# Kernel optimization log

Hardware: AMD Instinct MI355X
Metric: run time of the kernel (lower is better)

Reference implementation:

```python
import jax, jax.numpy as jnp
import numpy as np

N, CH = 65536, 256
B, K, CTX = 8, 256, 768
H, D = 8, 64
NPB = N // B  # points per batch (scene)


def setup_inputs() -> dict:
    key = jax.random.key(0)
    ks = jax.random.split(key, 8)
    xF = jax.random.normal(ks[0], (N, CH), dtype=jnp.float32)
    context = jax.random.normal(ks[1], (B, K, CTX), dtype=jnp.float32)
    # decomposition_permutations: a random partition of the N sparse points into B groups
    perm = jax.random.permutation(ks[2], N).reshape(B, NPB).astype(jnp.int32)
    Wq = jax.random.normal(ks[3], (CH, H * D), dtype=jnp.float32) * 0.02
    Wk = jax.random.normal(ks[4], (CTX, H * D), dtype=jnp.float32) * 0.02
    Wv = jax.random.normal(ks[5], (CTX, H * D), dtype=jnp.float32) * 0.02
    Wout = jax.random.normal(ks[6], (H * D, CH), dtype=jnp.float32) * 0.02
    b_out = jnp.zeros((CH,), dtype=jnp.float32)
    return {"xF": xF, "context": context, "perm": perm,
            "Wq": Wq, "Wk": Wk, "Wv": Wv, "Wout": Wout, "b_out": b_out}


def reference(xF, context, perm, Wq, Wk, Wv, Wout, b_out):
    scale = D ** -0.5
    q = (xF @ Wq).reshape(N, H, D)                     # to_q (1x1 conv == linear)
    k = (context @ Wk).reshape(B, K, H, D)             # to_k
    v = (context @ Wv).reshape(B, K, H, D)             # to_v
    qg = q[perm]                                        # gather: [B, NPB, H, D]
    attn = jax.nn.softmax(scale * jnp.einsum('bqhd,bkhd->bhqk', qg, k), axis=-1)
    o = jnp.einsum('bhqk,bkhd->bqhd', attn, v).reshape(B * NPB, H * D)
    # inverse-permutation scatter back to sparse-tensor order: ft[inv_perm]
    ft = jnp.zeros((N, H * D), o.dtype).at[perm.reshape(-1)].set(o)
    out = ft @ Wout + b_out                             # to_out
    return out + xF                                     # residual
```

## Files before the change

### kernel.cpp

```cpp
#include <hip/hip_runtime.h>

typedef unsigned short u16;
typedef __attribute__((ext_vector_type(8))) short bf16x8;
typedef __attribute__((ext_vector_type(4))) float f32x4;
typedef __attribute__((ext_vector_type(4))) int i32x4;
typedef __attribute__((ext_vector_type(2))) int i32x2;

#define N_PTS   65536
#define CH_DIM  256
#define BATCH   8
#define KTOK    256
#define CTX_DIM 768
#define NHEAD   8
#define HD      64
#define HDIM    512
#define NPB     8192

__device__ __forceinline__ u16 f2bf(float f) {
    union { float f; unsigned u; } v; v.f = f;
    unsigned r = v.u + 0x7fffu + ((v.u >> 16) & 1u);
    return (u16)(r >> 16);
}
__device__ __forceinline__ unsigned pk2bf(float lo, float hi) {
    return (unsigned)f2bf(lo) | ((unsigned)f2bf(hi) << 16);
}

__device__ __forceinline__ void gll16(const void* g, void* l) {
    __builtin_amdgcn_global_load_lds(
        (const __attribute__((address_space(1))) void*)g,
        (__attribute__((address_space(3))) void*)l, 16, 0, 0);
}

__global__ void convk(const float* __restrict__ src, u16* __restrict__ dst, int n8) {
    int i = blockIdx.x * blockDim.x + threadIdx.x;
    int st = gridDim.x * blockDim.x;
    for (; i < n8; i += st) {
        const float* p = src + (size_t)i * 8;
        f32x4 a = *(const f32x4*)p;
        f32x4 b = *(const f32x4*)(p + 4);
        union { u16 h[8]; i32x4 q; } pk;
#pragma unroll
        for (int j = 0; j < 4; j++) { pk.h[j] = f2bf(a[j]); pk.h[4 + j] = f2bf(b[j]); }
        *(i32x4*)&dst[(size_t)i * 8] = pk.q;
    }
}

__global__ void tconvk(const float* __restrict__ W, u16* __restrict__ WT, int R, int C) {
    int i = blockIdx.x * blockDim.x + threadIdx.x;
    if (i >= R * C) return;
    int c = i / R, r = i - c * R;
    WT[(size_t)c * R + r] = f2bf(W[(size_t)r * C + c]);
}

template <bool OUT_F32, bool VT_OUT>
__global__ __launch_bounds__(256, 3) void gemm_bt(
    const u16* __restrict__ A, const u16* __restrict__ BT, void* __restrict__ Cv,
    int M, int N, int K,
    const float* __restrict__ bias, const float* __restrict__ resid, float oscale)
{
    __shared__ __align__(16) u16 As[128 * 32];
    __shared__ __align__(16) u16 Bs[128 * 32];

    const int tid  = threadIdx.x;
    const int lane = tid & 63;
    const int w    = tid >> 6;
    const int wm   = w & 1;
    const int wn   = w >> 1;

    const int nwg = gridDim.x * gridDim.y;
    const int wg  = blockIdx.y * gridDim.x + blockIdx.x;
    const int swz = (wg & 7) * (nwg >> 3) + (wg >> 3);
    const int n0  = (swz % gridDim.x) * 128;
    const int m0  = (swz / gridDim.x) * 128;

    const int l15  = lane & 15;
    const int quad = lane >> 4;

    f32x4 acc[4][4];
#pragma unroll
    for (int i = 0; i < 4; i++)
#pragma unroll
        for (int j = 0; j < 4; j++) { acc[i][j][0]=0.f; acc[i][j][1]=0.f; acc[i][j][2]=0.f; acc[i][j][3]=0.f; }

    const int sr = tid >> 2;
    const int sc = (tid & 3) * 8;
    const u16* Abase = A  + (size_t)(m0 + sr) * K + sc;
    const u16* Bbase = BT + (size_t)(n0 + sr) * K + sc;
    u16* AsD = &As[tid * 8];
    u16* BsD = &Bs[tid * 8];
    const size_t rowStep = (size_t)64 * K;

    for (int k0 = 0; k0 < K; k0 += 32) {
        gll16(Abase + k0,           AsD);
        gll16(Abase + k0 + rowStep, AsD + 2048);
        gll16(Bbase + k0,           BsD);
        gll16(Bbase + k0 + rowStep, BsD + 2048);
        __syncthreads();

        bf16x8 af[4], bfr[4];
#pragma unroll
        for (int rt = 0; rt < 4; rt++)
            af[rt] = *(const bf16x8*)&As[(wm * 64 + rt * 16 + l15) * 32 + quad * 8];
#pragma unroll
        for (int nt = 0; nt < 4; nt++)
            bfr[nt] = *(const bf16x8*)&Bs[(wn * 64 + nt * 16 + l15) * 32 + quad * 8];
#pragma unroll
        for (int rt = 0; rt < 4; rt++)
#pragma unroll
            for (int nt = 0; nt < 4; nt++)
                acc[rt][nt] = __builtin_amdgcn_mfma_f32_16x16x32_bf16(af[rt], bfr[nt], acc[rt][nt], 0, 0, 0);
        __syncthreads();
    }

    if (VT_OUT) {
        u16* CT = (u16*)Cv;
#pragma unroll
        for (int nt = 0; nt < 4; nt++) {
            int col = n0 + wn * 64 + nt * 16 + l15;
            int hh = col >> 6, dd = col & 63;
#pragma unroll
            for (int rt = 0; rt < 4; rt++) {
                int row = m0 + wm * 64 + rt * 16 + quad * 4;
                int bb = row >> 8, jb = row & 255;
                int jp = (jb & 0xE0) | ((jb & 0x0C) << 1) | ((jb & 0x10) >> 2);
                union { u16 h[4]; i32x2 q; } pk;
#pragma unroll
                for (int r = 0; r < 4; r++) pk.h[r] = f2bf(acc[rt][nt][r]);
                *(i32x2*)&CT[(((size_t)(bb * 8 + hh)) * 64 + dd) * 256 + jp] = pk.q;
            }
        }
    } else {
#pragma unroll
        for (int nt = 0; nt < 4; nt++) {
            int col = n0 + wn * 64 + nt * 16 + l15;
            float bv = bias ? bias[col] : 0.0f;
#pragma unroll
            for (int rt = 0; rt < 4; rt++) {
#pragma unroll
                for (int r = 0; r < 4; r++) {
                    int row = m0 + wm * 64 + rt * 16 + quad * 4 + r;
                    float v = acc[rt][nt][r] + bv;
                    if (resid) v += resid[(size_t)row * N + col];
                    if (OUT_F32) ((float*)Cv)[(size_t)row * N + col] = v;
                    else         ((u16*)Cv)[(size_t)row * N + col]   = f2bf(v * oscale);
                }
            }
        }
    }
}

#define KS2 72
#define VS2 264
__global__ __launch_bounds__(256, 4) void attn_mfma(
    const u16* qbuf, const u16* __restrict__ kbuf,
    const u16* __restrict__ vbufT, const int* __restrict__ perm,
    u16* ft)
{
    __shared__ __align__(16) u16 smem[18432];
    u16* Ks = smem;
    u16* Vt = smem;

    const int tid   = threadIdx.x;
    const int lane  = tid & 63;
    const int w     = tid >> 6;
    const int chunk = blockIdx.x;
    const int bh    = blockIdx.y;
    const int b     = bh >> 3;
    const int h     = bh & 7;
    const int l15   = lane & 15;
    const int quad  = lane >> 4;

    const int prow = perm[b * NPB + chunk * 64 + w * 16 + l15];
    const u16* qrow = qbuf + (size_t)prow * HDIM + h * HD;
    bf16x8 qf0 = *(const bf16x8*)&qrow[quad * 8];
    bf16x8 qf1 = *(const bf16x8*)&qrow[32 + quad * 8];

    {
        const int j8 = tid >> 3;
        const int c  = (tid & 7) * 8;
#pragma unroll
        for (int pass = 0; pass < 8; pass++) {
            int jj = j8 + pass * 32;
            i32x4 val = *(const i32x4*)&kbuf[((size_t)(b * KTOK + jj)) * HDIM + h * HD + c];
            *(i32x4*)&Ks[jj * KS2 + c] = val;
        }
    }
    __syncthreads();

    f32x4 sc[16];
#pragma unroll
    for (int nt = 0; nt < 16; nt++) { sc[nt][0]=0.f; sc[nt][1]=0.f; sc[nt][2]=0.f; sc[nt][3]=0.f; }
#pragma unroll
    for (int nt = 0; nt < 16; nt++) {
        bf16x8 kf = *(const bf16x8*)&Ks[(nt * 16 + l15) * KS2 + quad * 8];
        sc[nt] = __builtin_amdgcn_mfma_f32_16x16x32_bf16(kf, qf0, sc[nt], 0, 0, 0);
    }
#pragma unroll
    for (int nt = 0; nt < 16; nt++) {
        bf16x8 kf = *(const bf16x8*)&Ks[(nt * 16 + l15) * KS2 + 32 + quad * 8];
        sc[nt] = __builtin_amdgcn_mfma_f32_16x16x32_bf16(kf, qf1, sc[nt], 0, 0, 0);
    }

    i32x4 vreg[8];
    const u16* vslice = vbufT + ((size_t)(b * NHEAD + h)) * HD * KTOK;
    const int vrow = tid >> 2;
    const int vc0  = (tid & 3) * 8;
#pragma unroll
    for (int pass = 0; pass < 8; pass++)
        vreg[pass] = *(const i32x4*)&vslice[(size_t)vrow * KTOK + vc0 + pass * 32];

    float m = -1e30f;
#pragma unroll
    for (int nt = 0; nt < 16; nt++) {
        f32x4 v = sc[nt];
        m = fmaxf(m, fmaxf(fmaxf(v[0], v[1]), fmaxf(v[2], v[3])));
    }
    m = fmaxf(m, __shfl_xor(m, 16));
    m = fmaxf(m, __shfl_xor(m, 32));
    float s = 0.f;
#pragma unroll
    for (int nt = 0; nt < 16; nt++) {
#pragma unroll
        for (int r = 0; r < 4; r++) { float e = __expf(sc[nt][r] - m); sc[nt][r] = e; s += e; }
    }
    s += __shfl_xor(s, 16);
    s += __shfl_xor(s, 32);
    float inv = 1.0f / s;

    unsigned up[16][2];
#pragma unroll
    for (int nt = 0; nt < 16; nt++) {
        up[nt][0] = pk2bf(sc[nt][0], sc[nt][1]);
        up[nt][1] = pk2bf(sc[nt][2], sc[nt][3]);
    }

    __syncthreads();

#pragma unroll
    for (int pass = 0; pass < 8; pass++)
        *(i32x4*)&Vt[vrow * VS2 + vc0 + pass * 32] = vreg[pass];
    __syncthreads();

    f32x4 o[4];
#pragma unroll
    for (int n = 0; n < 4; n++) { o[n][0]=0.f; o[n][1]=0.f; o[n][2]=0.f; o[n][3]=0.f; }

#pragma unroll
    for (int ks = 0; ks < 8; ks++) {
        union { unsigned u[4]; bf16x8 v; } pb;
        pb.u[0] = up[2 * ks][0];
        pb.u[1] = up[2 * ks][1];
        pb.u[2] = up[2 * ks + 1][0];
        pb.u[3] = up[2 * ks + 1][1];
#pragma unroll
        for (int nt = 0; nt < 4; nt++) {
            bf16x8 bv = *(const bf16x8*)&Vt[(nt * 16 + l15) * VS2 + ks * 32 + quad * 8];
            o[nt] = __builtin_amdgcn_mfma_f32_16x16x32_bf16(pb.v, bv, o[nt], 0, 0, 0);
        }
    }

#pragma unroll
    for (int r = 0; r < 4; r++) {
        float invq = __shfl(inv,  quad * 4 + r);
        int   po   = __shfl(prow, quad * 4 + r);
        u16* frow = ft + (size_t)po * HDIM + h * HD;
#pragma unroll
        for (int nt = 0; nt < 4; nt++)
            frow[nt * 16 + l15] = f2bf(o[nt][r] * invq);
    }
}

extern "C" void kernel_launch(void* const* d_in, const int* in_sizes, int n_in,
                              void* d_out, int out_size, void* d_ws, size_t ws_size,
                              hipStream_t stream) {
    const float* xF      = (const float*)d_in[0];
    const float* context = (const float*)d_in[1];
    const int*   perm    = (const int*)d_in[2];
    const float* Wq      = (const float*)d_in[3];
    const float* Wk      = (const float*)d_in[4];
    const float* Wv      = (const float*)d_in[5];
    const float* Wout    = (const float*)d_in[6];
    const float* b_out   = (const float*)d_in[7];
    float*       out     = (float*)d_out;

    const size_t WS_NEED = 71303168ULL;
    if (ws_size < WS_NEED) {
        hipMemsetAsync(d_out, 0, (size_t)out_size * sizeof(float), stream);
        return;
    }
    char* ws    = (char*)d_ws;
    u16* kbuf   = (u16*)(ws + 0);
    u16* vbufT  = (u16*)(ws + 2097152);
    u16* qbuf   = (u16*)(ws + 4194304);
    u16* ft     = qbuf;
    u16* WoutT  = (u16*)(ws + 2097152);

    char* ob    = (char*)d_out;
    u16* xb     = (u16*)(ob + 0);
    u16* cb     = (u16*)(ob + 33554432);
    u16* WqT    = (u16*)(ob + 36700160);
    u16* WkT    = (u16*)(ob + 36962304);
    u16* WvT    = (u16*)(ob + 37748736);

    convk<<<2048, 256, 0, stream>>>(xF, xb, N_PTS * CH_DIM / 8);
    convk<<<768, 256, 0, stream>>>(context, cb, BATCH * KTOK * CTX_DIM / 8);
    tconvk<<<(CH_DIM * HDIM + 255) / 256, 256, 0, stream>>>(Wq, WqT, CH_DIM, HDIM);
    tconvk<<<(CTX_DIM * HDIM + 255) / 256, 256, 0, stream>>>(Wk, WkT, CTX_DIM, HDIM);
    tconvk<<<(CTX_DIM * HDIM + 255) / 256, 256, 0, stream>>>(Wv, WvT, CTX_DIM, HDIM);

    gemm_bt<false, false><<<dim3(HDIM / 128, N_PTS / 128), 256, 0, stream>>>(
        xb, WqT, qbuf, N_PTS, HDIM, CH_DIM, nullptr, nullptr, 0.125f);
    gemm_bt<false, false><<<dim3(HDIM / 128, (BATCH * KTOK) / 128), 256, 0, stream>>>(
        cb, WkT, kbuf, BATCH * KTOK, HDIM, CTX_DIM, nullptr, nullptr, 1.0f);
    gemm_bt<false, true><<<dim3(HDIM / 128, (BATCH * KTOK) / 128), 256, 0, stream>>>(
        cb, WvT, vbufT, BATCH * KTOK, HDIM, CTX_DIM, nullptr, nullptr, 1.0f);

    attn_mfma<<<dim3(NPB / 64, BATCH * NHEAD), 256, 0, stream>>>(
        qbuf, kbuf, vbufT, perm, ft);

    tconvk<<<(HDIM * CH_DIM + 255) / 256, 256, 0, stream>>>(Wout, WoutT, HDIM, CH_DIM);
    gemm_bt<true, false><<<dim3(CH_DIM / 128, N_PTS / 128), 256, 0, stream>>>(
        ft, WoutT, out, N_PTS, CH_DIM, HDIM, b_out, xF, 1.0f);
}
```

Baseline: 331.3 us.

## Use hardware bf16 pack and exp2, fold log2e into Q scale, small-tile K/V GEMMs

Replaces software float-to-bf16 rounding with the v_cvt_pk_bf16_f32 instruction in the conversion, GEMM epilogue and attention kernels. Softmax now calls v_exp_f32 directly, with log2(e) folded into the Q projection scale, and sums with four independent accumulators. The K and V projection GEMMs move to a new 64x64-tile kernel so the small 2048-row problems launch more workgroups. This trims ALU work in the conversion and softmax paths and adds parallelism to the small GEMMs, at the cost of inline assembly tied to this ISA.

```diff
diff --git a/kernel.cpp b/kernel.cpp
--- a/kernel.cpp
+++ b/kernel.cpp
@@ -21,8 +21,15 @@
     unsigned r = v.u + 0x7fffu + ((v.u >> 16) & 1u);
     return (u16)(r >> 16);
 }
-__device__ __forceinline__ unsigned pk2bf(float lo, float hi) {
-    return (unsigned)f2bf(lo) | ((unsigned)f2bf(hi) << 16);
+__device__ __forceinline__ unsigned cvtpk(float lo, float hi) {
+    unsigned r;
+    asm("v_cvt_pk_bf16_f32 %0, %1, %2" : "=v"(r) : "v"(lo), "v"(hi));
+    return r;
+}
+__device__ __forceinline__ float exp2_hw(float x) {
+    float r;
+    asm("v_exp_f32 %0, %1" : "=v"(r) : "v"(x));
+    return r;
 }
 
 __device__ __forceinline__ void gll16(const void* g, void* l) {
@@ -38,10 +45,12 @@
         const float* p = src + (size_t)i * 8;
         f32x4 a = *(const f32x4*)p;
         f32x4 b = *(const f32x4*)(p + 4);
-        union { u16 h[8]; i32x4 q; } pk;
-#pragma unroll
-        for (int j = 0; j < 4; j++) { pk.h[j] = f2bf(a[j]); pk.h[4 + j] = f2bf(b[j]); }
-        *(i32x4*)&dst[(size_t)i * 8] = pk.q;
+        i32x4 o;
+        o[0] = (int)cvtpk(a[0], a[1]);
+        o[1] = (int)cvtpk(a[2], a[3]);
+        o[2] = (int)cvtpk(b[0], b[1]);
+        o[3] = (int)cvtpk(b[2], b[3]);
+        *(i32x4*)&dst[(size_t)i * 8] = o;
     }
 }
 
@@ -123,9 +132,9 @@
                 int row = m0 + wm * 64 + rt * 16 + quad * 4;
                 int bb = row >> 8, jb = row & 255;
                 int jp = (jb & 0xE0) | ((jb & 0x0C) << 1) | ((jb & 0x10) >> 2);
-                union { u16 h[4]; i32x2 q; } pk;
-#pragma unroll
-                for (int r = 0; r < 4; r++) pk.h[r] = f2bf(acc[rt][nt][r]);
+                union { unsigned u[2]; i32x2 q; } pk;
+                pk.u[0] = cvtpk(acc[rt][nt][0], acc[rt][nt][1]);
+                pk.u[1] = cvtpk(acc[rt][nt][2], acc[rt][nt][3]);
                 *(i32x2*)&CT[(((size_t)(bb * 8 + hh)) * 64 + dd) * 256 + jp] = pk.q;
             }
         }
@@ -139,6 +148,100 @@
 #pragma unroll
                 for (int r = 0; r < 4; r++) {
                     int row = m0 + wm * 64 + rt * 16 + quad * 4 + r;
+                    float v = acc[rt][nt][r] + bv;
+                    if (resid) v += resid[(size_t)row * N + col];
+                    if (OUT_F32) ((float*)Cv)[(size_t)row * N + col] = v;
+                    else         ((u16*)Cv)[(size_t)row * N + col]   = f2bf(v * oscale);
+                }
+            }
+        }
+    }
+}
+
+template <bool OUT_F32, bool VT_OUT>
+__global__ __launch_bounds__(256, 8) void gemm64(
+    const u16* __restrict__ A, const u16* __restrict__ BT, void* __restrict__ Cv,
+    int M, int N, int K,
+    const float* __restrict__ bias, const float* __restrict__ resid, float oscale)
+{
+    __shared__ __align__(16) u16 As[64 * 32];
+    __shared__ __align__(16) u16 Bs[64 * 32];
+
+    const int tid  = threadIdx.x;
+    const int lane = tid & 63;
+    const int w    = tid >> 6;
+    const int wm   = w & 1;
+    const int wn   = w >> 1;
+
+    const int nwg = gridDim.x * gridDim.y;
+    const int wg  = blockIdx.y * gridDim.x + blockIdx.x;
+    const int swz = (wg & 7) * (nwg >> 3) + (wg >> 3);
+    const int n0  = (swz % gridDim.x) * 64;
+    const int m0  = (swz / gridDim.x) * 64;
+
+    const int l15  = lane & 15;
+    const int quad = lane >> 4;
+
+    f32x4 acc[2][2];
+#pragma unroll
+    for (int i = 0; i < 2; i++)
+#pragma unroll
+        for (int j = 0; j < 2; j++) { acc[i][j][0]=0.f; acc[i][j][1]=0.f; acc[i][j][2]=0.f; acc[i][j][3]=0.f; }
+
+    const int sr = tid >> 2;
+    const int sc = (tid & 3) * 8;
+    const u16* Abase = A  + (size_t)(m0 + sr) * K + sc;
+    const u16* Bbase = BT + (size_t)(n0 + sr) * K + sc;
+    u16* AsD = &As[tid * 8];
+    u16* BsD = &Bs[tid * 8];
+
+    for (int k0 = 0; k0 < K; k0 += 32) {
+        gll16(Abase + k0, AsD);
+        gll16(Bbase + k0, BsD);
+        __syncthreads();
+
+        bf16x8 af[2], bfr[2];
+#pragma unroll
+        for (int rt = 0; rt < 2; rt++)
+            af[rt] = *(const bf16x8*)&As[(wm * 32 + rt * 16 + l15) * 32 + quad * 8];
+#pragma unroll
+        for (int nt = 0; nt < 2; nt++)
+            bfr[nt] = *(const bf16x8*)&Bs[(wn * 32 + nt * 16 + l15) * 32 + quad * 8];
+#pragma unroll
+        for (int rt = 0; rt < 2; rt++)
+#pragma unroll
+            for (int nt = 0; nt < 2; nt++)
+                acc[rt][nt] = __builtin_amdgcn_mfma_f32_16x16x32_bf16(af[rt], bfr[nt], acc[rt][nt], 0, 0, 0);
+        __syncthreads();
+    }
+
+    if (VT_OUT) {
+        u16* CT = (u16*)Cv;
+#pragma unroll
+        for (int nt = 0; nt < 2; nt++) {
+            int col = n0 + wn * 32 + nt * 16 + l15;
+            int hh = col >> 6, dd = col & 63;
+#pragma unroll
+            for (int rt = 0; rt < 2; rt++) {
+                int row = m0 + wm * 32 + rt * 16 + quad * 4;
+                int bb = row >> 8, jb = row & 255;
+                int jp = (jb & 0xE0) | ((jb & 0x0C) << 1) | ((jb & 0x10) >> 2);
+                union { unsigned u[2]; i32x2 q; } pk;
+                pk.u[0] = cvtpk(acc[rt][nt][0], acc[rt][nt][1]);
+                pk.u[1] = cvtpk(acc[rt][nt][2], acc[rt][nt][3]);
+                *(i32x2*)&CT[(((size_t)(bb * 8 + hh)) * 64 + dd) * 256 + jp] = pk.q;
+            }
+        }
+    } else {
+#pragma unroll
+        for (int nt = 0; nt < 2; nt++) {
+            int col = n0 + wn * 32 + nt * 16 + l15;
+            float bv = bias ? bias[col] : 0.0f;
+#pragma unroll
+            for (int rt = 0; rt < 2; rt++) {
+#pragma unroll
+                for (int r = 0; r < 4; r++) {
+                    int row = m0 + wm * 32 + rt * 16 + quad * 4 + r;
                     float v = acc[rt][nt][r] + bv;
                     if (resid) v += resid[(size_t)row * N + col];
                     if (OUT_F32) ((float*)Cv)[(size_t)row * N + col] = v;
@@ -217,12 +320,17 @@
     }
     m = fmaxf(m, __shfl_xor(m, 16));
     m = fmaxf(m, __shfl_xor(m, 32));
-    float s = 0.f;
+    float s0 = 0.f, s1 = 0.f, s2 = 0.f, s3 = 0.f;
 #pragma unroll
     for (int nt = 0; nt < 16; nt++) {
-#pragma unroll
-        for (int r = 0; r < 4; r++) { float e = __expf(sc[nt][r] - m); sc[nt][r] = e; s += e; }
-    }
+        float e0 = exp2_hw(sc[nt][0] - m);
+        float e1 = exp2_hw(sc[nt][1] - m);
+        float e2 = exp2_hw(sc[nt][2] - m);
+        float e3 = exp2_hw(sc[nt][3] - m);
+        sc[nt][0] = e0; sc[nt][1] = e1; sc[nt][2] = e2; sc[nt][3] = e3;
+        s0 += e0; s1 += e1; s2 += e2; s3 += e3;
+    }
+    float s = (s0 + s1) + (s2 + s3);
     s += __shfl_xor(s, 16);
     s += __shfl_xor(s, 32);
     float inv = 1.0f / s;
@@ -230,8 +338,8 @@
     unsigned up[16][2];
 #pragma unroll
     for (int nt = 0; nt < 16; nt++) {
-        up[nt][0] = pk2bf(sc[nt][0], sc[nt][1]);
-        up[nt][1] = pk2bf(sc[nt][2], sc[nt][3]);
+        up[nt][0] = cvtpk(sc[nt][0], sc[nt][1]);
+        up[nt][1] = cvtpk(sc[nt][2], sc[nt][3]);
     }
 
     __syncthreads();
@@ -264,9 +372,12 @@
         float invq = __shfl(inv,  quad * 4 + r);
         int   po   = __shfl(prow, quad * 4 + r);
         u16* frow = ft + (size_t)po * HDIM + h * HD;
-#pragma unroll
-        for (int nt = 0; nt < 4; nt++)
-            frow[nt * 16 + l15] = f2bf(o[nt][r] * invq);
+        unsigned pa = cvtpk(o[0][r] * invq, o[1][r] * invq);
+        unsigned pb = cvtpk(o[2][r] * invq, o[3][r] * invq);
+        frow[l15]      = (u16)pa;
+        frow[16 + l15] = (u16)(pa >> 16);
+        frow[32 + l15] = (u16)pb;
+        frow[48 + l15] = (u16)(pb >> 16);
     }
 }
 
@@ -309,10 +420,10 @@
     tconvk<<<(CTX_DIM * HDIM + 255) / 256, 256, 0, stream>>>(Wv, WvT, CTX_DIM, HDIM);
 
     gemm_bt<false, false><<<dim3(HDIM / 128, N_PTS / 128), 256, 0, stream>>>(
-        xb, WqT, qbuf, N_PTS, HDIM, CH_DIM, nullptr, nullptr, 0.125f);
-    gemm_bt<false, false><<<dim3(HDIM / 128, (BATCH * KTOK) / 128), 256, 0, stream>>>(
+        xb, WqT, qbuf, N_PTS, HDIM, CH_DIM, nullptr, nullptr, 0.1803368801f);
+    gemm64<false, false><<<dim3(HDIM / 64, (BATCH * KTOK) / 64), 256, 0, stream>>>(
         cb, WkT, kbuf, BATCH * KTOK, HDIM, CTX_DIM, nullptr, nullptr, 1.0f);
-    gemm_bt<false, true><<<dim3(HDIM / 128, (BATCH * KTOK) / 128), 256, 0, stream>>>(
+    gemm64<false, true><<<dim3(HDIM / 64, (BATCH * KTOK) / 64), 256, 0, stream>>>(
         cb, WvT, vbufT, BATCH * KTOK, HDIM, CTX_DIM, nullptr, nullptr, 1.0f);
 
     attn_mfma<<<dim3(NPB / 64, BATCH * NHEAD), 256, 0, stream>>>(
```

Result: faster. 302.2 us (-8.8%).
